# Kernel tuning notes

Hardware: AMD Instinct MI355X
Metric: run time of the kernel (lower is better)

Reference implementation:

```python
import jax, jax.numpy as jnp
import numpy as np

B, C, H, W = 64, 10, 30, 30
D, NH, HD = 64, 4, 16
EPS = 1e-5


def _conv(x, w, b):
    # x: [B,Cin,H,W], w: [Cout,Cin,kh,kw] (OIHW), SAME padding, stride 1
    y = jax.lax.conv_general_dilated(x, w, (1, 1), 'SAME',
                                     dimension_numbers=('NCHW', 'OIHW', 'NCHW'))
    return y + b[None, :, None, None]


def setup_inputs() -> dict:
    key = jax.random.key(0)
    ks = jax.random.split(key, 20)
    inp = {}
    inp['input_grid'] = jax.random.uniform(ks[0], (B, C, H, W), dtype=jnp.float32)
    inp['embed'] = jax.random.normal(ks[1], (10, D), dtype=jnp.float32)
    # MultiheadAttention packed in_proj [3D, D] and out_proj [D, D]
    inp['in_proj_w'] = jax.random.normal(ks[2], (3 * D, D), dtype=jnp.float32) * 0.08
    inp['in_proj_b'] = jnp.zeros((3 * D,), dtype=jnp.float32)
    inp['out_proj_w'] = jax.random.normal(ks[3], (D, D), dtype=jnp.float32) * 0.08
    inp['out_proj_b'] = jnp.zeros((D,), dtype=jnp.float32)
    # spatial encoder convs
    inp['conv1_w'] = jax.random.normal(ks[4], (32, 10, 3, 3), dtype=jnp.float32) * 0.1
    inp['conv1_b'] = jnp.zeros((32,), dtype=jnp.float32)
    inp['conv2_w'] = jax.random.normal(ks[5], (64, 32, 3, 3), dtype=jnp.float32) * 0.06
    inp['conv2_b'] = jnp.zeros((64,), dtype=jnp.float32)
    # color mapper MLP 64 -> 128 -> 100
    inp['lin1_w'] = jax.random.normal(ks[6], (128, 64), dtype=jnp.float32) * 0.1
    inp['lin1_b'] = jnp.zeros((128,), dtype=jnp.float32)
    inp['lin2_w'] = jax.random.normal(ks[7], (100, 128), dtype=jnp.float32) * 0.08
    inp['lin2_b'] = jnp.zeros((100,), dtype=jnp.float32)
    # decoder: ConvTranspose2d(64,32,3,pad=1) weight is [in=64,out=32,3,3]
    inp['dec1_w'] = jax.random.normal(ks[8], (64, 32, 3, 3), dtype=jnp.float32) * 0.06
    inp['dec1_b'] = jnp.zeros((32,), dtype=jnp.float32)
    inp['bn_g'] = jnp.ones((32,), dtype=jnp.float32)
    inp['bn_b'] = jnp.zeros((32,), dtype=jnp.float32)
    # ConvTranspose2d(32,10,1) weight [in=32,out=10,1,1] -> store as [32,10]
    inp['dec2_w'] = jax.random.normal(ks[9], (32, 10), dtype=jnp.float32) * 0.26
    inp['dec2_b'] = jnp.array([0.0, 0.08, 0.06, 0.07, 0.05, 0.06, 0.08, 0.09, 0.07, 0.06],
                              dtype=jnp.float32)
    return inp


def reference(input_grid, embed, in_proj_w, in_proj_b, out_proj_w, out_proj_b,
              conv1_w, conv1_b, conv2_w, conv2_b,
              lin1_w, lin1_b, lin2_w, lin2_b,
              dec1_w, dec1_b, bn_g, bn_b, dec2_w, dec2_b):
    b, c, h, w = input_grid.shape
    L = h * w
    idx = jnp.argmax(input_grid, axis=1)                      # [B,H,W] int
    x = embed[idx].reshape(b, L, D)                           # [B,L,64]

    # self-attention (torch MHA semantics, avg attn weights over heads)
    qkv = x @ in_proj_w.T + in_proj_b                         # [B,L,3D]
    q, k, v = jnp.split(qkv, 3, axis=-1)
    def heads(t):
        return t.reshape(b, L, NH, HD).transpose(0, 2, 1, 3)  # [B,NH,L,HD]
    q, k, v = heads(q), heads(k), heads(v)
    scores = jnp.einsum('bhqd,bhkd->bhqk', q, k) / np.sqrt(HD)
    attn = jax.nn.softmax(scores, axis=-1)                    # [B,NH,L,L]
    color_weights = attn.mean(axis=1)                         # [B,L,L]
    ctx = jnp.einsum('bhqk,bhkd->bhqd', attn, v)
    ctx = ctx.transpose(0, 2, 1, 3).reshape(b, L, D)
    attended = ctx @ out_proj_w.T + out_proj_b                # [B,L,64]
    attended_sp = attended.reshape(b, h, w, D).transpose(0, 3, 1, 2)  # [B,64,H,W]

    # spatial encoder
    s = jax.nn.relu(_conv(input_grid, conv1_w, conv1_b))
    s = jax.nn.relu(_conv(s, conv2_w, conv2_b))
    combined = s + attended_sp                                # [B,64,H,W]

    # global pool -> color map logits
    gf = combined.mean(axis=(2, 3))                           # [B,64]
    hmid = jax.nn.relu(gf @ lin1_w.T + lin1_b)
    color_map_logits = (hmid @ lin2_w.T + lin2_b).reshape(b, 10, 10)

    # vectorized color remap (replaces the per-batch/per-color scatter loop)
    new_color = jnp.argmax(color_map_logits, axis=-1)         # [B,10]
    pix = jnp.take_along_axis(new_color, idx.reshape(b, L), axis=1).reshape(b, h, w)
    mapped_output = jax.nn.one_hot(pix, 10, dtype=input_grid.dtype)
    mapped_output = mapped_output.transpose(0, 3, 1, 2)       # [B,10,H,W]

    # decoder: convT(64->32,k3,p1,s1) == conv with flipped kernel, SAME
    w1 = jnp.flip(dec1_w, axis=(2, 3)).transpose(1, 0, 2, 3)  # [32,64,3,3] OIHW
    d = _conv(combined, w1, dec1_b)
    # BatchNorm2d eval mode: running_mean=0, running_var=1
    d = d / np.sqrt(1.0 + EPS) * bn_g[None, :, None, None] + bn_b[None, :, None, None]
    d = jax.nn.relu(d)                                        # Dropout2d inactive (inference)
    predicted_output = jnp.einsum('bihw,io->bohw', d, dec2_w) + dec2_b[None, :, None, None]

    color_map = jax.nn.softmax(color_map_logits, axis=-1)
    return predicted_output, color_map, color_weights, mapped_output
```

## Files before the change

### kernel.cpp

```cpp
#include <hip/hip_runtime.h>
#include <cstddef>

#define B 64
#define NC 10
#define L 900
#define STASH_STRIDE 36000

typedef float f32x4 __attribute__((ext_vector_type(4)));

#define SCR_COMB   0
#define SCR_S1     3686400
#define SCR_AT     5529600
#define SCR_VE     5570560
#define SCR_S      5571200
#define SCR_WT2    5571600
#define SCR_WT1    5590032
#define SCR_BIAS1  5608464
#define SCR_GFP    5608496
#define SCR_CNT    5669936
#define SCR_FLOATS 5670576

__global__ __launch_bounds__(256) void k_front(
    const float* __restrict__ g, const float* __restrict__ embed,
    const float* __restrict__ ipw, const float* __restrict__ ipb,
    const float* __restrict__ cw1, const float* __restrict__ c1b,
    const float* __restrict__ cw2, const float* __restrict__ dw,
    const float* __restrict__ db, const float* __restrict__ bng,
    const float* __restrict__ bnb,
    float* __restrict__ scr, unsigned char* __restrict__ stash) {
  int bid = blockIdx.x, t = threadIdx.x;
  __shared__ float smem[4352];
  if (bid == 0) {
    float* emb = smem; float* q = smem + 640; float* k = smem + 1280;
    float* ve = scr + SCR_VE; float* S = scr + SCR_S;
    for (int i = t; i < 640; i += 256) emb[i] = embed[i];
    __syncthreads();
    for (int row = t; row < 192; row += 256) {
      int which = row >> 6, d = row & 63;
      for (int c = 0; c < 10; ++c) {
        float acc = ipb[row];
        for (int j = 0; j < 64; ++j) acc += emb[c * 64 + j] * ipw[row * 64 + j];
        if (which == 0) q[c * 64 + d] = acc;
        else if (which == 1) k[c * 64 + d] = acc;
        else ve[c * 64 + d] = acc;
      }
    }
    __syncthreads();
    for (int i = t; i < 400; i += 256) {
      int h = i / 100, r = i % 100, cq = r / 10, ck = r % 10;
      float acc = 0.f;
      for (int e = 0; e < 16; ++e)
        acc += q[cq * 64 + h * 16 + e] * k[ck * 64 + h * 16 + e];
      S[i] = acc * 0.25f;
    }
  } else if (bid <= 145) {
    int i = (bid - 1) * 256 + t;
    if (i < 18432) {
      int r = i / 64, oc = i % 64;
      scr[SCR_WT2 + r * 64 + oc] = cw2[oc * 288 + r];
    } else if (i < 36864) {
      int e = i - 18432, r = e / 32, oc = e % 32;
      int ic = r / 9, kk = r % 9, ky = kk / 3, kx = kk % 3;
      float s = bng[oc] / sqrtf(1.f + 1e-5f);
      scr[SCR_WT1 + r * 32 + oc] = dw[((ic * 32 + oc) * 3 + (2 - ky)) * 3 + (2 - kx)] * s;
    } else if (i < 36896) {
      int oc = i - 36864;
      float s = bng[oc] / sqrtf(1.f + 1e-5f);
      scr[SCR_BIAS1 + oc] = db[oc] * s + bnb[oc];
    }
  } else if (bid <= 209) {
    int b = bid - 146;
    int* hist = (int*)smem;
    int* cnt = (int*)(scr + SCR_CNT);
    if (t < 10) hist[t] = 0;
    __syncthreads();
    const float* gb = g + (size_t)b * NC * L;
    int* sidx = (int*)(stash + (size_t)b * STASH_STRIDE);
    for (int p = t; p < L; p += 256) {
      float best = gb[p]; int bi = 0;
      for (int c = 1; c < NC; ++c) {
        float v = gb[c * L + p];
        if (v > best) { best = v; bi = c; }
      }
      sidx[p] = bi;
      atomicAdd(&hist[bi], 1);
    }
    __syncthreads();
    if (t < 10) cnt[b * NC + t] = hist[t];
  } else {
    int blk = bid - 210, b = blk / 15, pr = blk % 15, oh0 = pr * 2;
    float* ins = smem;
    float* ws = smem + 1360;
    float* s1 = scr + SCR_S1;
    for (int i = t; i < 2880; i += 256) ws[i] = cw1[i];
    for (int e = t; e < 1360; e += 256) {
      int r = e / 340, rem = e % 340, ic = rem / 34, x = rem % 34;
      int y = oh0 + r - 1, gx = x - 1;
      float v = 0.f;
      if (y >= 0 && y < 30 && gx >= 0 && gx < 30)
        v = g[(size_t)(b * 10 + ic) * 900 + y * 30 + gx];
      ins[(r * 10 + ic) * 34 + x] = v;
    }
    __syncthreads();
    int lane = t & 63, ow = lane & 31, rr = lane >> 5;
    int oc0 = __builtin_amdgcn_readfirstlane((t >> 6) * 8);
    float acc[8];
    #pragma unroll
    for (int j = 0; j < 8; ++j) acc[j] = c1b[oc0 + j];
    for (int ic = 0; ic < 10; ++ic) {
      #pragma unroll
      for (int ky = 0; ky < 3; ++ky) {
        #pragma unroll
        for (int kx = 0; kx < 3; ++kx) {
          float iv = ins[((rr + ky) * 10 + ic) * 34 + ow + kx];
          #pragma unroll
          for (int j = 0; j < 8; ++j)
            acc[j] = fmaf(iv, ws[((oc0 + j) * 10 + ic) * 9 + ky * 3 + kx], acc[j]);
        }
      }
    }
    if (ow < 30) {
      #pragma unroll
      for (int j = 0; j < 8; ++j)
        s1[(size_t)(b * 32 + oc0 + j) * 900 + (oh0 + rr) * 30 + ow] = fmaxf(acc[j], 0.f);
    }
  }
}

__global__ void k_attn(const float* __restrict__ S, const float* __restrict__ ve,
                       const int* __restrict__ cnt,
                       const float* __restrict__ opw, const float* __restrict__ opb,
                       float* __restrict__ AT, unsigned char* __restrict__ stash) {
  int b = blockIdx.x, t = threadIdx.x;
  float* scw = (float*)(stash + (size_t)b * STASH_STRIDE + 3640);
  __shared__ float A[4][10][10];
  __shared__ float cf[10];
  __shared__ float ctx[10][64];
  if (t < 10) cf[t] = (float)cnt[b * 10 + t];
  __syncthreads();
  if (t < 40) {
    int h = t / 10, cq = t % 10;
    const float* Sr = S + (h * 10 + cq) * 10;
    float m = -1e30f;
    for (int c = 0; c < 10; ++c) if (cf[c] > 0.f) m = fmaxf(m, Sr[c]);
    float e[10]; float Z = 0.f;
    for (int c = 0; c < 10; ++c) { e[c] = expf(Sr[c] - m); Z += cf[c] * e[c]; }
    float inv = 1.f / Z;
    for (int c = 0; c < 10; ++c) A[h][cq][c] = e[c] * inv;
  }
  __syncthreads();
  if (t < 100) {
    int cq = t / 10, ck = t % 10;
    scw[t] = 0.25f * (A[0][cq][ck] + A[1][cq][ck] + A[2][cq][ck] + A[3][cq][ck]);
  }
  for (int i = t; i < 640; i += 128) {
    int cq = i >> 6, dd = i & 63, h = dd >> 4;
    float acc = 0.f;
    for (int ck = 0; ck < 10; ++ck) acc += A[h][cq][ck] * cf[ck] * ve[ck * 64 + dd];
    ctx[cq][dd] = acc;
  }
  __syncthreads();
  for (int i = t; i < 640; i += 128) {
    int cq = i >> 6, dd = i & 63;
    float acc = opb[dd];
    for (int e = 0; e < 64; ++e) acc += ctx[cq][e] * opw[dd * 64 + e];
    AT[(b * 10 + cq) * 64 + dd] = acc;
  }
}

__global__ __launch_bounds__(256) void k_c2(const float* __restrict__ scr_s1,
                                            const float* __restrict__ wt2,
                                            const float* __restrict__ cb,
                                            const float* __restrict__ AT,
                                            const unsigned char* __restrict__ stash,
                                            float* __restrict__ comb,
                                            float* __restrict__ gfp) {
  int blk = blockIdx.x, b = blk / 15, pr = blk % 15, oh0 = pr * 2;
  int t = threadIdx.x;
  __shared__ float ins[4][32][34];
  for (int e = t; e < 4352; e += 256) {
    int r = e / 1088, rem = e % 1088, ic = rem / 34, x = rem % 34;
    int y = oh0 + r - 1, gx = x - 1;
    float v = 0.f;
    if (y >= 0 && y < 30 && gx >= 0 && gx < 30)
      v = scr_s1[(size_t)(b * 32 + ic) * 900 + y * 30 + gx];
    ins[r][ic][x] = v;
  }
  __syncthreads();
  int lane = t & 63, ow = lane & 31, rr = lane >> 5;
  int oc0 = __builtin_amdgcn_readfirstlane((t >> 6) * 16);
  float acc[16];
  #pragma unroll
  for (int j = 0; j < 16; ++j) acc[j] = cb[oc0 + j];
  for (int ic = 0; ic < 32; ++ic) {
    #pragma unroll
    for (int ky = 0; ky < 3; ++ky) {
      #pragma unroll
      for (int kx = 0; kx < 3; ++kx) {
        float iv = ins[rr + ky][ic][ow + kx];
        const float* wr = wt2 + (ic * 9 + ky * 3 + kx) * 64 + oc0;
        #pragma unroll
        for (int j = 0; j < 16; ++j) acc[j] = fmaf(iv, wr[j], acc[j]);
      }
    }
  }
  float outv[16];
  if (ow < 30) {
    const int* sidx = (const int*)(stash + (size_t)b * STASH_STRIDE);
    int c = sidx[(oh0 + rr) * 30 + ow];
    const float* at = AT + ((size_t)b * 10 + c) * 64 + oc0;
    #pragma unroll
    for (int j = 0; j < 16; ++j) {
      outv[j] = fmaxf(acc[j], 0.f) + at[j];
      comb[(size_t)(b * 64 + oc0 + j) * 900 + (oh0 + rr) * 30 + ow] = outv[j];
    }
  } else {
    #pragma unroll
    for (int j = 0; j < 16; ++j) outv[j] = 0.f;
  }
  #pragma unroll
  for (int j = 0; j < 16; ++j) {
    float v = outv[j];
    for (int o = 32; o; o >>= 1) v += __shfl_down(v, o, 64);
    if (lane == 0) gfp[(b * 15 + pr) * 64 + oc0 + j] = v;
  }
}

__global__ __launch_bounds__(256) void k_back(
    const float* __restrict__ scr,
    const float* __restrict__ l1w, const float* __restrict__ l1b,
    const float* __restrict__ l2w, const float* __restrict__ l2b,
    const float* __restrict__ w2, const float* __restrict__ b2,
    float* __restrict__ out_pred, float* __restrict__ out_cm,
    float* __restrict__ out_cw2, unsigned char* __restrict__ stash) {
  int bid = blockIdx.x, t = threadIdx.x;
  __shared__ float smem[10880];
  if (bid < 64) {
    int b = bid;
    float* gfl = smem; float* hmid = smem + 64; float* lg = smem + 192;
    const float* gfp = scr + SCR_GFP;
    if (t < 64) {
      float a = 0.f;
      for (int pr = 0; pr < 15; ++pr) a += gfp[(b * 15 + pr) * 64 + t];
      gfl[t] = a * (1.f / 900.f);
    }
    __syncthreads();
    if (t < 128) {
      float acc = l1b[t];
      for (int j = 0; j < 64; ++j) acc += gfl[j] * l1w[t * 64 + j];
      hmid[t] = fmaxf(acc, 0.f);
    }
    __syncthreads();
    if (t < 100) {
      float acc = l2b[t];
      for (int j = 0; j < 128; ++j) acc += hmid[j] * l2w[t * 128 + j];
      lg[t] = acc;
    }
    __syncthreads();
    if (t < 10) {
      float m = lg[t * 10]; int am = 0;
      for (int j = 1; j < 10; ++j) {
        float v = lg[t * 10 + j];
        if (v > m) { m = v; am = j; }
      }
      float e[10]; float Z = 0.f;
      for (int j = 0; j < 10; ++j) { e[j] = expf(lg[t * 10 + j] - m); Z += e[j]; }
      float inv = 1.f / Z;
      for (int j = 0; j < 10; ++j) out_cm[(b * 10 + t) * 10 + j] = e[j] * inv;
      ((int*)(stash + (size_t)b * STASH_STRIDE + 3600))[t] = am;
    }
  } else if (bid < 1024) {
    int blk = bid - 64, b = blk / 15, pr = blk % 15, oh0 = pr * 2;
    float* ins = smem;
    float* d1s = smem + 8704;
    const float* comb = scr + SCR_COMB;
    const float* wt1 = scr + SCR_WT1;
    const float* bias1 = scr + SCR_BIAS1;
    for (int e = t; e < 8704; e += 256) {
      int r = e / 2176, rem = e % 2176, ic = rem / 34, x = rem % 34;
      int y = oh0 + r - 1, gx = x - 1;
      float v = 0.f;
      if (y >= 0 && y < 30 && gx >= 0 && gx < 30)
        v = comb[(size_t)(b * 64 + ic) * 900 + y * 30 + gx];
      ins[(r * 64 + ic) * 34 + x] = v;
    }
    __syncthreads();
    int lane = t & 63, ow = lane & 31, rr = lane >> 5;
    int oc0 = __builtin_amdgcn_readfirstlane((t >> 6) * 8);
    float acc[8];
    #pragma unroll
    for (int j = 0; j < 8; ++j) acc[j] = bias1[oc0 + j];
    for (int ic = 0; ic < 64; ++ic) {
      #pragma unroll
      for (int ky = 0; ky < 3; ++ky) {
        #pragma unroll
        for (int kx = 0; kx < 3; ++kx) {
          float iv = ins[((rr + ky) * 64 + ic) * 34 + ow + kx];
          const float* wr = wt1 + (ic * 9 + ky * 3 + kx) * 32 + oc0;
          #pragma unroll
          for (int j = 0; j < 8; ++j) acc[j] = fmaf(iv, wr[j], acc[j]);
        }
      }
    }
    if (ow < 30) {
      #pragma unroll
      for (int j = 0; j < 8; ++j) d1s[(rr * 32 + oc0 + j) * 32 + ow] = fmaxf(acc[j], 0.f);
    }
    __syncthreads();
    for (int e = t; e < 600; e += 256) {
      int r = e / 300, rem = e % 300, o = rem / 30, ow2 = rem % 30;
      float a2 = b2[o];
      #pragma unroll
      for (int ic = 0; ic < 32; ++ic) a2 += d1s[(r * 32 + ic) * 32 + ow2] * w2[ic * 10 + o];
      out_pred[(size_t)(b * 10 + o) * 900 + (oh0 + r) * 30 + ow2] = a2;
    }
  } else {
    int blk = bid - 1024, b = blk / 60, rc = blk % 60;
    float* lut = smem;
    float* cwb = smem + 9000;
    unsigned char* cols = (unsigned char*)(smem + 9100);
    const unsigned char* sl = stash + (size_t)b * STASH_STRIDE;
    const int* sidx = (const int*)sl;
    const float* scw = (const float*)(sl + 3640);
    for (int i = t; i < 900; i += 256) cols[i] = (unsigned char)sidx[i];
    for (int i = t; i < 100; i += 256) cwb[i] = scw[i];
    __syncthreads();
    for (int i = t; i < 9000; i += 256) {
      int cq = i / 900, p = i % 900;
      lut[cq * 900 + p] = cwb[cq * 10 + cols[p]];
    }
    __syncthreads();
    int base = rc * 15;
    for (int i = t; i < 15 * 225; i += 256) {
      int r = i / 225, ch = i % 225;
      int p = base + r;
      int cq = cols[p];
      f32x4 v = *(const f32x4*)&lut[cq * 900 + ch * 4];
      __builtin_nontemporal_store(v, (f32x4*)&out_cw2[(size_t)b * 810000 + (size_t)p * 900 + ch * 4]);
    }
  }
}

__global__ void k_cw(const unsigned char* __restrict__ stash,
                     float* __restrict__ out2) {
  int blk = blockIdx.x;
  int b = blk / 60, rc = blk % 60;
  int t = threadIdx.x;
  const unsigned char* sl = stash + (size_t)b * STASH_STRIDE;
  const int* sidx = (const int*)sl;
  const float* scw = (const float*)(sl + 3640);
  __shared__ float lut[10][900];
  __shared__ unsigned char cols[900];
  __shared__ float cwb[100];
  for (int i = t; i < 900; i += 256) cols[i] = (unsigned char)sidx[i];
  for (int i = t; i < 100; i += 256) cwb[i] = scw[i];
  __syncthreads();
  for (int i = t; i < 9000; i += 256) {
    int cq = i / 900, p = i % 900;
    lut[cq][p] = cwb[cq * 10 + cols[p]];
  }
  __syncthreads();
  int base = rc * 15;
  for (int i = t; i < 15 * 225; i += 256) {
    int r = i / 225, ch = i % 225;
    int p = base + r;
    int cq = cols[p];
    f32x4 v = *(const f32x4*)&lut[cq][ch * 4];
    __builtin_nontemporal_store(v, (f32x4*)&out2[(size_t)b * 810000 + (size_t)p * 900 + ch * 4]);
  }
}

__global__ void k_map(const unsigned char* __restrict__ stash,
                      float* __restrict__ out4) {
  int b = blockIdx.x, t = threadIdx.x;
  const unsigned char* sl = stash + (size_t)b * STASH_STRIDE;
  const int* sidx = (const int*)sl;
  const int* sncol = (const int*)(sl + 3600);
  __shared__ unsigned char scol[900];
  __shared__ int sn[10];
  for (int i = t; i < 900; i += 256) scol[i] = (unsigned char)sidx[i];
  if (t < 10) sn[t] = sncol[t];
  __syncthreads();
  for (int i = t; i < 9000; i += 256) {
    int ch = i / 900, p = i % 900;
    out4[(size_t)b * 9000 + i] = (sn[scol[p]] == ch) ? 1.0f : 0.0f;
  }
}

extern "C" void kernel_launch(void* const* d_in, const int* in_sizes, int n_in,
                              void* d_out, int out_size, void* d_ws, size_t ws_size,
                              hipStream_t stream) {
  const float* input_grid = (const float*)d_in[0];
  const float* embed      = (const float*)d_in[1];
  const float* in_proj_w  = (const float*)d_in[2];
  const float* in_proj_b  = (const float*)d_in[3];
  const float* out_proj_w = (const float*)d_in[4];
  const float* out_proj_b = (const float*)d_in[5];
  const float* conv1_w    = (const float*)d_in[6];
  const float* conv1_b    = (const float*)d_in[7];
  const float* conv2_w    = (const float*)d_in[8];
  const float* conv2_b    = (const float*)d_in[9];
  const float* lin1_w     = (const float*)d_in[10];
  const float* lin1_b     = (const float*)d_in[11];
  const float* lin2_w     = (const float*)d_in[12];
  const float* lin2_b     = (const float*)d_in[13];
  const float* dec1_w     = (const float*)d_in[14];
  const float* dec1_b     = (const float*)d_in[15];
  const float* bn_g       = (const float*)d_in[16];
  const float* bn_b       = (const float*)d_in[17];
  const float* dec2_w     = (const float*)d_in[18];
  const float* dec2_b     = (const float*)d_in[19];

  float* out      = (float*)d_out;
  float* out_pred = out;
  float* out_cmap = out + 576000;
  float* out_cw   = out + 582400;
  float* out_map  = out + 52422400;

  bool ws_ok = ws_size >= (size_t)SCR_FLOATS * 4;
  float* scr = ws_ok ? (float*)d_ws : out_cw;
  unsigned char* stash = (unsigned char*)out_map;

  k_front<<<1170, 256, 0, stream>>>(input_grid, embed, in_proj_w, in_proj_b,
                                    conv1_w, conv1_b, conv2_w, dec1_w, dec1_b,
                                    bn_g, bn_b, scr, stash);
  k_attn<<<B, 128, 0, stream>>>(scr + SCR_S, scr + SCR_VE, (int*)(scr + SCR_CNT),
                                out_proj_w, out_proj_b, scr + SCR_AT, stash);
  k_c2<<<960, 256, 0, stream>>>(scr + SCR_S1, scr + SCR_WT2, conv2_b,
                                scr + SCR_AT, stash, scr + SCR_COMB, scr + SCR_GFP);
  k_back<<<ws_ok ? 4864 : 1024, 256, 0, stream>>>(scr, lin1_w, lin1_b, lin2_w, lin2_b,
                                                  dec2_w, dec2_b, out_pred, out_cmap,
                                                  out_cw, stash);
  if (!ws_ok) k_cw<<<B * 60, 256, 0, stream>>>(stash, out_cw);
  k_map<<<B, 256, 0, stream>>>(stash, out_map);
}
```

Baseline: 179.3 us.

## Fuse attention into conv2 kernel and mapped-output into back kernel

The per-batch attention work is folded into the conv2 kernel: each conv2 block recomputes its batch's softmax, context and output projection into shared memory instead of reading a separate AT buffer. A new branch in k_back recomputes the colour-mapper MLP argmax and writes the one-hot mapped output, so k_map is dropped. The workspace layout is reorganised, with s1 placed in the color_weights output region and the stash moved into the workspace. The default path goes from five launches to three, at the cost of redundant attention math in every conv2 block (15x per batch) and a duplicated MLP.

```diff
diff --git a/kernel.cpp b/kernel.cpp
--- a/kernel.cpp
+++ b/kernel.cpp
@@ -4,21 +4,8 @@
 #define B 64
 #define NC 10
 #define L 900
-#define STASH_STRIDE 36000
 
 typedef float f32x4 __attribute__((ext_vector_type(4)));
-
-#define SCR_COMB   0
-#define SCR_S1     3686400
-#define SCR_AT     5529600
-#define SCR_VE     5570560
-#define SCR_S      5571200
-#define SCR_WT2    5571600
-#define SCR_WT1    5590032
-#define SCR_BIAS1  5608464
-#define SCR_GFP    5608496
-#define SCR_CNT    5669936
-#define SCR_FLOATS 5670576
 
 __global__ __launch_bounds__(256) void k_front(
     const float* __restrict__ g, const float* __restrict__ embed,
@@ -27,12 +14,15 @@
     const float* __restrict__ cw2, const float* __restrict__ dw,
     const float* __restrict__ db, const float* __restrict__ bng,
     const float* __restrict__ bnb,
-    float* __restrict__ scr, unsigned char* __restrict__ stash) {
+    float* __restrict__ ve_g, float* __restrict__ S_g,
+    float* __restrict__ wt2, float* __restrict__ wt1,
+    float* __restrict__ bias1, int* __restrict__ cnt,
+    float* __restrict__ s1, unsigned char* __restrict__ stash,
+    int sstride) {
   int bid = blockIdx.x, t = threadIdx.x;
   __shared__ float smem[4352];
   if (bid == 0) {
     float* emb = smem; float* q = smem + 640; float* k = smem + 1280;
-    float* ve = scr + SCR_VE; float* S = scr + SCR_S;
     for (int i = t; i < 640; i += 256) emb[i] = embed[i];
     __syncthreads();
     for (int row = t; row < 192; row += 256) {
@@ -42,7 +32,7 @@
         for (int j = 0; j < 64; ++j) acc += emb[c * 64 + j] * ipw[row * 64 + j];
         if (which == 0) q[c * 64 + d] = acc;
         else if (which == 1) k[c * 64 + d] = acc;
-        else ve[c * 64 + d] = acc;
+        else ve_g[c * 64 + d] = acc;
       }
     }
     __syncthreads();
@@ -51,31 +41,30 @@
       float acc = 0.f;
       for (int e = 0; e < 16; ++e)
         acc += q[cq * 64 + h * 16 + e] * k[ck * 64 + h * 16 + e];
-      S[i] = acc * 0.25f;
+      S_g[i] = acc * 0.25f;
     }
   } else if (bid <= 145) {
     int i = (bid - 1) * 256 + t;
     if (i < 18432) {
       int r = i / 64, oc = i % 64;
-      scr[SCR_WT2 + r * 64 + oc] = cw2[oc * 288 + r];
+      wt2[r * 64 + oc] = cw2[oc * 288 + r];
     } else if (i < 36864) {
       int e = i - 18432, r = e / 32, oc = e % 32;
       int ic = r / 9, kk = r % 9, ky = kk / 3, kx = kk % 3;
       float s = bng[oc] / sqrtf(1.f + 1e-5f);
-      scr[SCR_WT1 + r * 32 + oc] = dw[((ic * 32 + oc) * 3 + (2 - ky)) * 3 + (2 - kx)] * s;
+      wt1[r * 32 + oc] = dw[((ic * 32 + oc) * 3 + (2 - ky)) * 3 + (2 - kx)] * s;
     } else if (i < 36896) {
       int oc = i - 36864;
       float s = bng[oc] / sqrtf(1.f + 1e-5f);
-      scr[SCR_BIAS1 + oc] = db[oc] * s + bnb[oc];
+      bias1[oc] = db[oc] * s + bnb[oc];
     }
   } else if (bid <= 209) {
     int b = bid - 146;
     int* hist = (int*)smem;
-    int* cnt = (int*)(scr + SCR_CNT);
     if (t < 10) hist[t] = 0;
     __syncthreads();
     const float* gb = g + (size_t)b * NC * L;
-    int* sidx = (int*)(stash + (size_t)b * STASH_STRIDE);
+    int* sidx = (int*)(stash + (size_t)b * sstride);
     for (int p = t; p < L; p += 256) {
       float best = gb[p]; int bi = 0;
       for (int c = 1; c < NC; ++c) {
@@ -91,7 +80,6 @@
     int blk = bid - 210, b = blk / 15, pr = blk % 15, oh0 = pr * 2;
     float* ins = smem;
     float* ws = smem + 1360;
-    float* s1 = scr + SCR_S1;
     for (int i = t; i < 2880; i += 256) ws[i] = cw1[i];
     for (int e = t; e < 1360; e += 256) {
       int r = e / 340, rem = e % 340, ic = rem / 34, x = rem % 34;
@@ -127,15 +115,28 @@
   }
 }
 
-__global__ void k_attn(const float* __restrict__ S, const float* __restrict__ ve,
-                       const int* __restrict__ cnt,
-                       const float* __restrict__ opw, const float* __restrict__ opb,
-                       float* __restrict__ AT, unsigned char* __restrict__ stash) {
-  int b = blockIdx.x, t = threadIdx.x;
-  float* scw = (float*)(stash + (size_t)b * STASH_STRIDE + 3640);
+__global__ __launch_bounds__(256) void k_c2attn(
+    const float* __restrict__ s1, const float* __restrict__ wt2,
+    const float* __restrict__ cb, const float* __restrict__ S,
+    const float* __restrict__ ve, const int* __restrict__ cnt,
+    const float* __restrict__ opw, const float* __restrict__ opb,
+    unsigned char* __restrict__ stash, int sstride,
+    float* __restrict__ comb, float* __restrict__ gfp) {
+  int blk = blockIdx.x, b = blk / 15, pr = blk % 15, oh0 = pr * 2;
+  int t = threadIdx.x;
+  __shared__ float ins[4][32][34];
   __shared__ float A[4][10][10];
   __shared__ float cf[10];
-  __shared__ float ctx[10][64];
+  __shared__ float ctx[10][65];
+  __shared__ float at[10][65];
+  for (int e = t; e < 4352; e += 256) {
+    int r = e / 1088, rem = e % 1088, ic = rem / 34, x = rem % 34;
+    int y = oh0 + r - 1, gx = x - 1;
+    float v = 0.f;
+    if (y >= 0 && y < 30 && gx >= 0 && gx < 30)
+      v = s1[(size_t)(b * 32 + ic) * 900 + y * 30 + gx];
+    ins[r][ic][x] = v;
+  }
   if (t < 10) cf[t] = (float)cnt[b * 10 + t];
   __syncthreads();
   if (t < 40) {
@@ -151,6 +152,86 @@
   __syncthreads();
   if (t < 100) {
     int cq = t / 10, ck = t % 10;
+    float* scw = (float*)(stash + (size_t)b * sstride + 3640);
+    scw[t] = 0.25f * (A[0][cq][ck] + A[1][cq][ck] + A[2][cq][ck] + A[3][cq][ck]);
+  }
+  for (int i = t; i < 640; i += 256) {
+    int cq = i >> 6, dd = i & 63, h = dd >> 4;
+    float acc = 0.f;
+    for (int ck = 0; ck < 10; ++ck) acc += A[h][cq][ck] * cf[ck] * ve[ck * 64 + dd];
+    ctx[cq][dd] = acc;
+  }
+  __syncthreads();
+  for (int i = t; i < 640; i += 256) {
+    int cq = i >> 6, dd = i & 63;
+    float acc = opb[dd];
+    for (int e = 0; e < 64; ++e) acc += ctx[cq][e] * opw[dd * 64 + e];
+    at[cq][dd] = acc;
+  }
+  __syncthreads();
+  int lane = t & 63, ow = lane & 31, rr = lane >> 5;
+  int oc0 = __builtin_amdgcn_readfirstlane((t >> 6) * 16);
+  float acc[16];
+  #pragma unroll
+  for (int j = 0; j < 16; ++j) acc[j] = cb[oc0 + j];
+  for (int ic = 0; ic < 32; ++ic) {
+    #pragma unroll
+    for (int ky = 0; ky < 3; ++ky) {
+      #pragma unroll
+      for (int kx = 0; kx < 3; ++kx) {
+        float iv = ins[rr + ky][ic][ow + kx];
+        const float* wr = wt2 + (ic * 9 + ky * 3 + kx) * 64 + oc0;
+        #pragma unroll
+        for (int j = 0; j < 16; ++j) acc[j] = fmaf(iv, wr[j], acc[j]);
+      }
+    }
+  }
+  float outv[16];
+  if (ow < 30) {
+    const int* sidx = (const int*)(stash + (size_t)b * sstride);
+    int c = sidx[(oh0 + rr) * 30 + ow];
+    #pragma unroll
+    for (int j = 0; j < 16; ++j) {
+      outv[j] = fmaxf(acc[j], 0.f) + at[c][oc0 + j];
+      comb[(size_t)(b * 64 + oc0 + j) * 900 + (oh0 + rr) * 30 + ow] = outv[j];
+    }
+  } else {
+    #pragma unroll
+    for (int j = 0; j < 16; ++j) outv[j] = 0.f;
+  }
+  #pragma unroll
+  for (int j = 0; j < 16; ++j) {
+    float v = outv[j];
+    for (int o = 32; o; o >>= 1) v += __shfl_down(v, o, 64);
+    if (lane == 0) gfp[(b * 15 + pr) * 64 + oc0 + j] = v;
+  }
+}
+
+__global__ void k_attn(const float* __restrict__ S, const float* __restrict__ ve,
+                       const int* __restrict__ cnt,
+                       const float* __restrict__ opw, const float* __restrict__ opb,
+                       float* __restrict__ AT, unsigned char* __restrict__ stash,
+                       int sstride) {
+  int b = blockIdx.x, t = threadIdx.x;
+  float* scw = (float*)(stash + (size_t)b * sstride + 3640);
+  __shared__ float A[4][10][10];
+  __shared__ float cf[10];
+  __shared__ float ctx[10][64];
+  if (t < 10) cf[t] = (float)cnt[b * 10 + t];
+  __syncthreads();
+  if (t < 40) {
+    int h = t / 10, cq = t % 10;
+    const float* Sr = S + (h * 10 + cq) * 10;
+    float m = -1e30f;
+    for (int c = 0; c < 10; ++c) if (cf[c] > 0.f) m = fmaxf(m, Sr[c]);
+    float e[10]; float Z = 0.f;
+    for (int c = 0; c < 10; ++c) { e[c] = expf(Sr[c] - m); Z += cf[c] * e[c]; }
+    float inv = 1.f / Z;
+    for (int c = 0; c < 10; ++c) A[h][cq][c] = e[c] * inv;
+  }
+  __syncthreads();
+  if (t < 100) {
+    int cq = t / 10, ck = t % 10;
     scw[t] = 0.25f * (A[0][cq][ck] + A[1][cq][ck] + A[2][cq][ck] + A[3][cq][ck]);
   }
   for (int i = t; i < 640; i += 128) {
@@ -168,11 +249,12 @@
   }
 }
 
-__global__ __launch_bounds__(256) void k_c2(const float* __restrict__ scr_s1,
+__global__ __launch_bounds__(256) void k_c2(const float* __restrict__ s1,
                                             const float* __restrict__ wt2,
                                             const float* __restrict__ cb,
                                             const float* __restrict__ AT,
                                             const unsigned char* __restrict__ stash,
+                                            int sstride,
                                             float* __restrict__ comb,
                                             float* __restrict__ gfp) {
   int blk = blockIdx.x, b = blk / 15, pr = blk % 15, oh0 = pr * 2;
@@ -183,7 +265,7 @@
     int y = oh0 + r - 1, gx = x - 1;
     float v = 0.f;
     if (y >= 0 && y < 30 && gx >= 0 && gx < 30)
-      v = scr_s1[(size_t)(b * 32 + ic) * 900 + y * 30 + gx];
+      v = s1[(size_t)(b * 32 + ic) * 900 + y * 30 + gx];
     ins[r][ic][x] = v;
   }
   __syncthreads();
@@ -206,12 +288,12 @@
   }
   float outv[16];
   if (ow < 30) {
-    const int* sidx = (const int*)(stash + (size_t)b * STASH_STRIDE);
+    const int* sidx = (const int*)(stash + (size_t)b * sstride);
     int c = sidx[(oh0 + rr) * 30 + ow];
-    const float* at = AT + ((size_t)b * 10 + c) * 64 + oc0;
+    const float* atp = AT + ((size_t)b * 10 + c) * 64 + oc0;
     #pragma unroll
     for (int j = 0; j < 16; ++j) {
-      outv[j] = fmaxf(acc[j], 0.f) + at[j];
+      outv[j] = fmaxf(acc[j], 0.f) + atp[j];
       comb[(size_t)(b * 64 + oc0 + j) * 900 + (oh0 + rr) * 30 + ow] = outv[j];
     }
   } else {
@@ -227,18 +309,19 @@
 }
 
 __global__ __launch_bounds__(256) void k_back(
-    const float* __restrict__ scr,
+    const float* __restrict__ comb, const float* __restrict__ wt1,
+    const float* __restrict__ bias1, const float* __restrict__ gfp,
     const float* __restrict__ l1w, const float* __restrict__ l1b,
     const float* __restrict__ l2w, const float* __restrict__ l2b,
     const float* __restrict__ w2, const float* __restrict__ b2,
     float* __restrict__ out_pred, float* __restrict__ out_cm,
-    float* __restrict__ out_cw2, unsigned char* __restrict__ stash) {
+    float* __restrict__ out_cw2, float* __restrict__ out_map,
+    unsigned char* __restrict__ stash, int sstride) {
   int bid = blockIdx.x, t = threadIdx.x;
   __shared__ float smem[10880];
   if (bid < 64) {
     int b = bid;
     float* gfl = smem; float* hmid = smem + 64; float* lg = smem + 192;
-    const float* gfp = scr + SCR_GFP;
     if (t < 64) {
       float a = 0.f;
       for (int pr = 0; pr < 15; ++pr) a += gfp[(b * 15 + pr) * 64 + t];
@@ -267,15 +350,12 @@
       for (int j = 0; j < 10; ++j) { e[j] = expf(lg[t * 10 + j] - m); Z += e[j]; }
       float inv = 1.f / Z;
       for (int j = 0; j < 10; ++j) out_cm[(b * 10 + t) * 10 + j] = e[j] * inv;
-      ((int*)(stash + (size_t)b * STASH_STRIDE + 3600))[t] = am;
+      ((int*)(stash + (size_t)b * sstride + 3600))[t] = am;
     }
   } else if (bid < 1024) {
     int blk = bid - 64, b = blk / 15, pr = blk % 15, oh0 = pr * 2;
     float* ins = smem;
     float* d1s = smem + 8704;
-    const float* comb = scr + SCR_COMB;
-    const float* wt1 = scr + SCR_WT1;
-    const float* bias1 = scr + SCR_BIAS1;
     for (int e = t; e < 8704; e += 256) {
       int r = e / 2176, rem = e % 2176, ic = rem / 34, x = rem % 34;
       int y = oh0 + r - 1, gx = x - 1;
@@ -314,12 +394,12 @@
       for (int ic = 0; ic < 32; ++ic) a2 += d1s[(r * 32 + ic) * 32 + ow2] * w2[ic * 10 + o];
       out_pred[(size_t)(b * 10 + o) * 900 + (oh0 + r) * 30 + ow2] = a2;
     }
-  } else {
+  } else if (bid < 4864) {
     int blk = bid - 1024, b = blk / 60, rc = blk % 60;
     float* lut = smem;
     float* cwb = smem + 9000;
     unsigned char* cols = (unsigned char*)(smem + 9100);
-    const unsigned char* sl = stash + (size_t)b * STASH_STRIDE;
+    const unsigned char* sl = stash + (size_t)b * sstride;
     const int* sidx = (const int*)sl;
     const float* scw = (const float*)(sl + 3640);
     for (int i = t; i < 900; i += 256) cols[i] = (unsigned char)sidx[i];
@@ -338,15 +418,53 @@
       f32x4 v = *(const f32x4*)&lut[cq * 900 + ch * 4];
       __builtin_nontemporal_store(v, (f32x4*)&out_cw2[(size_t)b * 810000 + (size_t)p * 900 + ch * 4]);
     }
-  }
-}
-
-__global__ void k_cw(const unsigned char* __restrict__ stash,
+  } else {
+    int b = bid - 4864;
+    float* gfl = smem; float* hmid = smem + 64; float* lg = smem + 192;
+    int* sn = (int*)(smem + 292);
+    unsigned char* scol = (unsigned char*)(smem + 302);
+    const int* sidx = (const int*)(stash + (size_t)b * sstride);
+    for (int i = t; i < 900; i += 256) scol[i] = (unsigned char)sidx[i];
+    if (t < 64) {
+      float a = 0.f;
+      for (int pr = 0; pr < 15; ++pr) a += gfp[(b * 15 + pr) * 64 + t];
+      gfl[t] = a * (1.f / 900.f);
+    }
+    __syncthreads();
+    if (t < 128) {
+      float acc = l1b[t];
+      for (int j = 0; j < 64; ++j) acc += gfl[j] * l1w[t * 64 + j];
+      hmid[t] = fmaxf(acc, 0.f);
+    }
+    __syncthreads();
+    if (t < 100) {
+      float acc = l2b[t];
+      for (int j = 0; j < 128; ++j) acc += hmid[j] * l2w[t * 128 + j];
+      lg[t] = acc;
+    }
+    __syncthreads();
+    if (t < 10) {
+      float m = lg[t * 10]; int am = 0;
+      for (int j = 1; j < 10; ++j) {
+        float v = lg[t * 10 + j];
+        if (v > m) { m = v; am = j; }
+      }
+      sn[t] = am;
+    }
+    __syncthreads();
+    for (int i = t; i < 9000; i += 256) {
+      int ch = i / 900, p = i % 900;
+      out_map[(size_t)b * 9000 + i] = (sn[scol[p]] == ch) ? 1.0f : 0.0f;
+    }
+  }
+}
+
+__global__ void k_cw(const unsigned char* __restrict__ stash, int sstride,
                      float* __restrict__ out2) {
   int blk = blockIdx.x;
   int b = blk / 60, rc = blk % 60;
   int t = threadIdx.x;
-  const unsigned char* sl = stash + (size_t)b * STASH_STRIDE;
+  const unsigned char* sl = stash + (size_t)b * sstride;
   const int* sidx = (const int*)sl;
   const float* scw = (const float*)(sl + 3640);
   __shared__ float lut[10][900];
@@ -370,10 +488,10 @@
   }
 }
 
-__global__ void k_map(const unsigned char* __restrict__ stash,
+__global__ void k_map(const unsigned char* __restrict__ stash, int sstride,
                       float* __restrict__ out4) {
   int b = blockIdx.x, t = threadIdx.x;
-  const unsigned char* sl = stash + (size_t)b * STASH_STRIDE;
+  const unsigned char* sl = stash + (size_t)b * sstride;
   const int* sidx = (const int*)sl;
   const int* sncol = (const int*)(sl + 3600);
   __shared__ unsigned char scol[900];
@@ -417,20 +535,59 @@
   float* out_cw   = out + 582400;
   float* out_map  = out + 52422400;
 
-  bool ws_ok = ws_size >= (size_t)SCR_FLOATS * 4;
-  float* scr = ws_ok ? (float*)d_ws : out_cw;
-  unsigned char* stash = (unsigned char*)out_map;
-
-  k_front<<<1170, 256, 0, stream>>>(input_grid, embed, in_proj_w, in_proj_b,
-                                    conv1_w, conv1_b, conv2_w, dec1_w, dec1_b,
-                                    bn_g, bn_b, scr, stash);
-  k_attn<<<B, 128, 0, stream>>>(scr + SCR_S, scr + SCR_VE, (int*)(scr + SCR_CNT),
-                                out_proj_w, out_proj_b, scr + SCR_AT, stash);
-  k_c2<<<960, 256, 0, stream>>>(scr + SCR_S1, scr + SCR_WT2, conv2_b,
-                                scr + SCR_AT, stash, scr + SCR_COMB, scr + SCR_GFP);
-  k_back<<<ws_ok ? 4864 : 1024, 256, 0, stream>>>(scr, lin1_w, lin1_b, lin2_w, lin2_b,
-                                                  dec2_w, dec2_b, out_pred, out_cmap,
-                                                  out_cw, stash);
-  if (!ws_ok) k_cw<<<B * 60, 256, 0, stream>>>(stash, out_cw);
-  k_map<<<B, 256, 0, stream>>>(stash, out_map);
-}
+  const size_t WS_NEED = (size_t)(3786416 + 65536) * 4;
+  bool ws_ok = ws_size >= WS_NEED;
+
+  if (ws_ok) {
+    float* w = (float*)d_ws;
+    float* comb  = w;
+    float* ve    = w + 3686400;
+    float* S     = w + 3687040;
+    float* wt2   = w + 3687440;
+    float* wt1   = w + 3705872;
+    float* bias1 = w + 3724304;
+    float* gfp   = w + 3724336;
+    int*   cnt   = (int*)(w + 3785776);
+    unsigned char* stash = (unsigned char*)(w + 3786416);
+    float* s1 = out_cw;
+
+    k_front<<<1170, 256, 0, stream>>>(input_grid, embed, in_proj_w, in_proj_b,
+                                      conv1_w, conv1_b, conv2_w, dec1_w, dec1_b,
+                                      bn_g, bn_b, ve, S, wt2, wt1, bias1, cnt,
+                                      s1, stash, 4096);
+    k_c2attn<<<960, 256, 0, stream>>>(s1, wt2, conv2_b, S, ve, cnt,
+                                      out_proj_w, out_proj_b, stash, 4096,
+                                      comb, gfp);
+    k_back<<<4928, 256, 0, stream>>>(comb, wt1, bias1, gfp, lin1_w, lin1_b,
+                                     lin2_w, lin2_b, dec2_w, dec2_b,
+                                     out_pred, out_cmap, out_cw, out_map,
+                                     stash, 4096);
+  } else {
+    float* scr = out_cw;
+    float* comb  = scr;
+    float* s1    = scr + 3686400;
+    float* AT    = scr + 5529600;
+    float* ve    = scr + 5570560;
+    float* S     = scr + 5571200;
+    float* wt2   = scr + 5571600;
+    float* wt1   = scr + 5590032;
+    float* bias1 = scr + 5608464;
+    float* gfp   = scr + 5608496;
+    int*   cnt   = (int*)(scr + 5669936);
+    unsigned char* stash = (unsigned char*)out_map;
+
+    k_front<<<1170, 256, 0, stream>>>(input_grid, embed, in_proj_w, in_proj_b,
+                                      conv1_w, conv1_b, conv2_w, dec1_w, dec1_b,
+                                      bn_g, bn_b, ve, S, wt2, wt1, bias1, cnt,
+                                      s1, stash, 36000);
+    k_attn<<<B, 128, 0, stream>>>(S, ve, cnt, out_proj_w, out_proj_b, AT,
+                                  stash, 36000);
+    k_c2<<<960, 256, 0, stream>>>(s1, wt2, conv2_b, AT, stash, 36000, comb, gfp);
+    k_back<<<1024, 256, 0, stream>>>(comb, wt1, bias1, gfp, lin1_w, lin1_b,
+                                     lin2_w, lin2_b, dec2_w, dec2_b,
+                                     out_pred, out_cmap, out_cw, out_map,
+                                     stash, 36000);
+    k_cw<<<B * 60, 256, 0, stream>>>(stash, 36000, out_cw);
+    k_map<<<B, 256, 0, stream>>>(stash, 36000, out_map);
+  }
+}
```

After: 180.1 us. No clear change (+0.5%).

## Fuse attention into conv2, recompute color weights per block, merge tail kernels

Applied to the files above, without the earlier changes.

The per-batch attention kernel is folded into the conv2 kernel, and each block now recomputes the attention context it needs into shared memory. The color-weight broadcast blocks recompute argmax, histogram, QK scores and softmax themselves instead of reading stashed values. They are interleaved with the decoder blocks in k_back, and the map output is computed there too. Scratch now lives in the tail of the color-weight output region, which is overwritten last by a separate tail kernel. This cuts kernel launches and dependencies and overlaps write-heavy work with decoder compute, at the cost of redundant recomputation in every block and an ordering dependence on scratch aliasing.

```diff
diff --git a/kernel.cpp b/kernel.cpp
--- a/kernel.cpp
+++ b/kernel.cpp
@@ -4,21 +4,101 @@
 #define B 64
 #define NC 10
 #define L 900
-#define STASH_STRIDE 36000
+#define SSTRIDE 36000
 
 typedef float f32x4 __attribute__((ext_vector_type(4)));
 
 #define SCR_COMB   0
 #define SCR_S1     3686400
-#define SCR_AT     5529600
-#define SCR_VE     5570560
-#define SCR_S      5571200
-#define SCR_WT2    5571600
-#define SCR_WT1    5590032
-#define SCR_BIAS1  5608464
-#define SCR_GFP    5608496
-#define SCR_CNT    5669936
-#define SCR_FLOATS 5670576
+#define SCR_VE     5529600
+#define SCR_S      5530240
+#define SCR_WT2    5530640
+#define SCR_WT1    5549072
+#define SCR_BIAS1  5567504
+#define SCR_GFP    5567536
+#define SCR_CNT    5628976
+
+__device__ __forceinline__ void cw_block(int b, int rc,
+                                         const float* __restrict__ g,
+                                         const float* __restrict__ embed,
+                                         const float* __restrict__ ipw,
+                                         const float* __restrict__ ipb,
+                                         float* __restrict__ out_cw,
+                                         float* sm) {
+  float* qs = sm;
+  float* ks = sm + 640;
+  float* Sl = sm + 1280;
+  float* lut = sm + 1680;
+  float* emb = sm + 1680;
+  float* cwb = sm + 10680;
+  float* cf = sm + 10780;
+  int* hist = (int*)(sm + 10790);
+  unsigned char* cols = (unsigned char*)(sm + 10800);
+  int t = threadIdx.x;
+  for (int i = t; i < 640; i += 256) emb[i] = embed[i];
+  if (t < 10) hist[t] = 0;
+  __syncthreads();
+  {
+    int row = t & 127, c0 = (t >> 7) * 5;
+    const float* wrow = ipw + row * 64;
+    float bias = ipb[row];
+    for (int c = c0; c < c0 + 5; ++c) {
+      float acc = bias;
+      for (int j = 0; j < 64; ++j) acc += emb[c * 64 + j] * wrow[j];
+      if (row < 64) qs[c * 64 + row] = acc;
+      else ks[c * 64 + (row - 64)] = acc;
+    }
+  }
+  const float* gb = g + (size_t)b * NC * L;
+  for (int p = t; p < 900; p += 256) {
+    float best = gb[p]; int bi = 0;
+    for (int c = 1; c < NC; ++c) {
+      float v = gb[c * L + p];
+      if (v > best) { best = v; bi = c; }
+    }
+    cols[p] = (unsigned char)bi;
+    atomicAdd(&hist[bi], 1);
+  }
+  __syncthreads();
+  for (int i = t; i < 400; i += 256) {
+    int h = i / 100, r = i % 100, cq = r / 10, ck = r % 10;
+    float acc = 0.f;
+    for (int e = 0; e < 16; ++e)
+      acc += qs[cq * 64 + h * 16 + e] * ks[ck * 64 + h * 16 + e];
+    Sl[i] = acc * 0.25f;
+  }
+  if (t < 10) cf[t] = (float)hist[t];
+  __syncthreads();
+  float* Al = qs;
+  if (t < 40) {
+    int h = t / 10, cq = t % 10;
+    const float* Sr = Sl + h * 100 + cq * 10;
+    float m = -1e30f;
+    for (int c = 0; c < 10; ++c) if (cf[c] > 0.f) m = fmaxf(m, Sr[c]);
+    float e[10]; float Z = 0.f;
+    for (int c = 0; c < 10; ++c) { e[c] = expf(Sr[c] - m); Z += cf[c] * e[c]; }
+    float inv = 1.f / Z;
+    for (int c = 0; c < 10; ++c) Al[(h * 10 + cq) * 10 + c] = e[c] * inv;
+  }
+  __syncthreads();
+  if (t < 100) {
+    cwb[t] = 0.25f * (Al[t] + Al[100 + t] + Al[200 + t] + Al[300 + t]);
+  }
+  __syncthreads();
+  for (int i = t; i < 9000; i += 256) {
+    int cq = i / 900, p = i % 900;
+    lut[cq * 900 + p] = cwb[cq * 10 + cols[p]];
+  }
+  __syncthreads();
+  int base = rc * 15;
+  for (int i = t; i < 15 * 225; i += 256) {
+    int r = i / 225, ch = i % 225;
+    int p = base + r;
+    int cq = cols[p];
+    f32x4 v = *(const f32x4*)&lut[cq * 900 + ch * 4];
+    __builtin_nontemporal_store(v, (f32x4*)&out_cw[(size_t)b * 810000 + (size_t)p * 900 + ch * 4]);
+  }
+}
 
 __global__ __launch_bounds__(256) void k_front(
     const float* __restrict__ g, const float* __restrict__ embed,
@@ -32,7 +112,6 @@
   __shared__ float smem[4352];
   if (bid == 0) {
     float* emb = smem; float* q = smem + 640; float* k = smem + 1280;
-    float* ve = scr + SCR_VE; float* S = scr + SCR_S;
     for (int i = t; i < 640; i += 256) emb[i] = embed[i];
     __syncthreads();
     for (int row = t; row < 192; row += 256) {
@@ -42,7 +121,7 @@
         for (int j = 0; j < 64; ++j) acc += emb[c * 64 + j] * ipw[row * 64 + j];
         if (which == 0) q[c * 64 + d] = acc;
         else if (which == 1) k[c * 64 + d] = acc;
-        else ve[c * 64 + d] = acc;
+        else scr[SCR_VE + c * 64 + d] = acc;
       }
     }
     __syncthreads();
@@ -51,7 +130,7 @@
       float acc = 0.f;
       for (int e = 0; e < 16; ++e)
         acc += q[cq * 64 + h * 16 + e] * k[ck * 64 + h * 16 + e];
-      S[i] = acc * 0.25f;
+      scr[SCR_S + i] = acc * 0.25f;
     }
   } else if (bid <= 145) {
     int i = (bid - 1) * 256 + t;
@@ -75,7 +154,7 @@
     if (t < 10) hist[t] = 0;
     __syncthreads();
     const float* gb = g + (size_t)b * NC * L;
-    int* sidx = (int*)(stash + (size_t)b * STASH_STRIDE);
+    int* sidx = (int*)(stash + (size_t)b * SSTRIDE);
     for (int p = t; p < L; p += 256) {
       float best = gb[p]; int bi = 0;
       for (int c = 1; c < NC; ++c) {
@@ -127,15 +206,30 @@
   }
 }
 
-__global__ void k_attn(const float* __restrict__ S, const float* __restrict__ ve,
-                       const int* __restrict__ cnt,
-                       const float* __restrict__ opw, const float* __restrict__ opb,
-                       float* __restrict__ AT, unsigned char* __restrict__ stash) {
-  int b = blockIdx.x, t = threadIdx.x;
-  float* scw = (float*)(stash + (size_t)b * STASH_STRIDE + 3640);
+__global__ __launch_bounds__(256) void k_c2attn(
+    const float* __restrict__ scr_in, const float* __restrict__ cb,
+    const float* __restrict__ opw, const float* __restrict__ opb,
+    const unsigned char* __restrict__ stash,
+    float* __restrict__ scr) {
+  int blk = blockIdx.x, b = blk / 15, pr = blk % 15, oh0 = pr * 2;
+  int t = threadIdx.x;
+  const float* s1 = scr_in + SCR_S1;
+  const float* S = scr_in + SCR_S;
+  const float* ve = scr_in + SCR_VE;
+  const int* cnt = (const int*)(scr_in + SCR_CNT);
+  __shared__ float ins[4][32][34];
   __shared__ float A[4][10][10];
   __shared__ float cf[10];
-  __shared__ float ctx[10][64];
+  __shared__ float ctx[10][65];
+  __shared__ float at[10][65];
+  for (int e = t; e < 4352; e += 256) {
+    int r = e / 1088, rem = e % 1088, ic = rem / 34, x = rem % 34;
+    int y = oh0 + r - 1, gx = x - 1;
+    float v = 0.f;
+    if (y >= 0 && y < 30 && gx >= 0 && gx < 30)
+      v = s1[(size_t)(b * 32 + ic) * 900 + y * 30 + gx];
+    ins[r][ic][x] = v;
+  }
   if (t < 10) cf[t] = (float)cnt[b * 10 + t];
   __syncthreads();
   if (t < 40) {
@@ -149,42 +243,18 @@
     for (int c = 0; c < 10; ++c) A[h][cq][c] = e[c] * inv;
   }
   __syncthreads();
-  if (t < 100) {
-    int cq = t / 10, ck = t % 10;
-    scw[t] = 0.25f * (A[0][cq][ck] + A[1][cq][ck] + A[2][cq][ck] + A[3][cq][ck]);
-  }
-  for (int i = t; i < 640; i += 128) {
+  for (int i = t; i < 640; i += 256) {
     int cq = i >> 6, dd = i & 63, h = dd >> 4;
     float acc = 0.f;
     for (int ck = 0; ck < 10; ++ck) acc += A[h][cq][ck] * cf[ck] * ve[ck * 64 + dd];
     ctx[cq][dd] = acc;
   }
   __syncthreads();
-  for (int i = t; i < 640; i += 128) {
+  for (int i = t; i < 640; i += 256) {
     int cq = i >> 6, dd = i & 63;
     float acc = opb[dd];
     for (int e = 0; e < 64; ++e) acc += ctx[cq][e] * opw[dd * 64 + e];
-    AT[(b * 10 + cq) * 64 + dd] = acc;
-  }
-}
-
-__global__ __launch_bounds__(256) void k_c2(const float* __restrict__ scr_s1,
-                                            const float* __restrict__ wt2,
-                                            const float* __restrict__ cb,
-                                            const float* __restrict__ AT,
-                                            const unsigned char* __restrict__ stash,
-                                            float* __restrict__ comb,
-                                            float* __restrict__ gfp) {
-  int blk = blockIdx.x, b = blk / 15, pr = blk % 15, oh0 = pr * 2;
-  int t = threadIdx.x;
-  __shared__ float ins[4][32][34];
-  for (int e = t; e < 4352; e += 256) {
-    int r = e / 1088, rem = e % 1088, ic = rem / 34, x = rem % 34;
-    int y = oh0 + r - 1, gx = x - 1;
-    float v = 0.f;
-    if (y >= 0 && y < 30 && gx >= 0 && gx < 30)
-      v = scr_s1[(size_t)(b * 32 + ic) * 900 + y * 30 + gx];
-    ins[r][ic][x] = v;
+    at[cq][dd] = acc;
   }
   __syncthreads();
   int lane = t & 63, ow = lane & 31, rr = lane >> 5;
@@ -192,6 +262,7 @@
   float acc[16];
   #pragma unroll
   for (int j = 0; j < 16; ++j) acc[j] = cb[oc0 + j];
+  const float* wt2 = scr_in + SCR_WT2;
   for (int ic = 0; ic < 32; ++ic) {
     #pragma unroll
     for (int ky = 0; ky < 3; ++ky) {
@@ -205,13 +276,13 @@
     }
   }
   float outv[16];
+  float* comb = scr + SCR_COMB;
   if (ow < 30) {
-    const int* sidx = (const int*)(stash + (size_t)b * STASH_STRIDE);
+    const int* sidx = (const int*)(stash + (size_t)b * SSTRIDE);
     int c = sidx[(oh0 + rr) * 30 + ow];
-    const float* at = AT + ((size_t)b * 10 + c) * 64 + oc0;
     #pragma unroll
     for (int j = 0; j < 16; ++j) {
-      outv[j] = fmaxf(acc[j], 0.f) + at[j];
+      outv[j] = fmaxf(acc[j], 0.f) + at[c][oc0 + j];
       comb[(size_t)(b * 64 + oc0 + j) * 900 + (oh0 + rr) * 30 + ow] = outv[j];
     }
   } else {
@@ -222,55 +293,33 @@
   for (int j = 0; j < 16; ++j) {
     float v = outv[j];
     for (int o = 32; o; o >>= 1) v += __shfl_down(v, o, 64);
-    if (lane == 0) gfp[(b * 15 + pr) * 64 + oc0 + j] = v;
+    if (lane == 0) scr[SCR_GFP + (b * 15 + pr) * 64 + oc0 + j] = v;
   }
 }
 
 __global__ __launch_bounds__(256) void k_back(
+    const float* __restrict__ g, const float* __restrict__ embed,
+    const float* __restrict__ ipw, const float* __restrict__ ipb,
     const float* __restrict__ scr,
     const float* __restrict__ l1w, const float* __restrict__ l1b,
     const float* __restrict__ l2w, const float* __restrict__ l2b,
     const float* __restrict__ w2, const float* __restrict__ b2,
     float* __restrict__ out_pred, float* __restrict__ out_cm,
-    float* __restrict__ out_cw2, unsigned char* __restrict__ stash) {
+    float* __restrict__ out_cw2, float* __restrict__ out_map,
+    unsigned char* __restrict__ stash) {
   int bid = blockIdx.x, t = threadIdx.x;
-  __shared__ float smem[10880];
-  if (bid < 64) {
-    int b = bid;
-    float* gfl = smem; float* hmid = smem + 64; float* lg = smem + 192;
-    const float* gfp = scr + SCR_GFP;
-    if (t < 64) {
-      float a = 0.f;
-      for (int pr = 0; pr < 15; ++pr) a += gfp[(b * 15 + pr) * 64 + t];
-      gfl[t] = a * (1.f / 900.f);
-    }
-    __syncthreads();
-    if (t < 128) {
-      float acc = l1b[t];
-      for (int j = 0; j < 64; ++j) acc += gfl[j] * l1w[t * 64 + j];
-      hmid[t] = fmaxf(acc, 0.f);
-    }
-    __syncthreads();
-    if (t < 100) {
-      float acc = l2b[t];
-      for (int j = 0; j < 128; ++j) acc += hmid[j] * l2w[t * 128 + j];
-      lg[t] = acc;
-    }
-    __syncthreads();
-    if (t < 10) {
-      float m = lg[t * 10]; int am = 0;
-      for (int j = 1; j < 10; ++j) {
-        float v = lg[t * 10 + j];
-        if (v > m) { m = v; am = j; }
-      }
-      float e[10]; float Z = 0.f;
-      for (int j = 0; j < 10; ++j) { e[j] = expf(lg[t * 10 + j] - m); Z += e[j]; }
-      float inv = 1.f / Z;
-      for (int j = 0; j < 10; ++j) out_cm[(b * 10 + t) * 10 + j] = e[j] * inv;
-      ((int*)(stash + (size_t)b * STASH_STRIDE + 3600))[t] = am;
-    }
-  } else if (bid < 1024) {
-    int blk = bid - 64, b = blk / 15, pr = blk % 15, oh0 = pr * 2;
+  __shared__ float smem[11100];
+  int cwid = -1, d1id = -1;
+  if (bid < 3840) {
+    if ((bid & 3) == 3) d1id = bid >> 2;
+    else cwid = (bid >> 2) * 3 + (bid & 3);
+  } else if (bid < 4320) {
+    cwid = 2880 + (bid - 3840);
+  }
+  if (cwid >= 0) {
+    cw_block(cwid / 60, cwid % 60, g, embed, ipw, ipb, out_cw2, smem);
+  } else if (d1id >= 0) {
+    int b = d1id / 15, pr = d1id % 15, oh0 = pr * 2;
     float* ins = smem;
     float* d1s = smem + 8704;
     const float* comb = scr + SCR_COMB;
@@ -314,77 +363,85 @@
       for (int ic = 0; ic < 32; ++ic) a2 += d1s[(r * 32 + ic) * 32 + ow2] * w2[ic * 10 + o];
       out_pred[(size_t)(b * 10 + o) * 900 + (oh0 + r) * 30 + ow2] = a2;
     }
+  } else if (bid < 4384) {
+    int b = bid - 4320;
+    float* gfl = smem; float* hmid = smem + 64; float* lg = smem + 192;
+    const float* gfp = scr + SCR_GFP;
+    if (t < 64) {
+      float a = 0.f;
+      for (int pr = 0; pr < 15; ++pr) a += gfp[(b * 15 + pr) * 64 + t];
+      gfl[t] = a * (1.f / 900.f);
+    }
+    __syncthreads();
+    if (t < 128) {
+      float acc = l1b[t];
+      for (int j = 0; j < 64; ++j) acc += gfl[j] * l1w[t * 64 + j];
+      hmid[t] = fmaxf(acc, 0.f);
+    }
+    __syncthreads();
+    if (t < 100) {
+      float acc = l2b[t];
+      for (int j = 0; j < 128; ++j) acc += hmid[j] * l2w[t * 128 + j];
+      lg[t] = acc;
+    }
+    __syncthreads();
+    if (t < 10) {
+      float m = lg[t * 10];
+      for (int j = 1; j < 10; ++j) m = fmaxf(m, lg[t * 10 + j]);
+      float e[10]; float Z = 0.f;
+      for (int j = 0; j < 10; ++j) { e[j] = expf(lg[t * 10 + j] - m); Z += e[j]; }
+      float inv = 1.f / Z;
+      for (int j = 0; j < 10; ++j) out_cm[(b * 10 + t) * 10 + j] = e[j] * inv;
+    }
   } else {
-    int blk = bid - 1024, b = blk / 60, rc = blk % 60;
-    float* lut = smem;
-    float* cwb = smem + 9000;
-    unsigned char* cols = (unsigned char*)(smem + 9100);
-    const unsigned char* sl = stash + (size_t)b * STASH_STRIDE;
-    const int* sidx = (const int*)sl;
-    const float* scw = (const float*)(sl + 3640);
-    for (int i = t; i < 900; i += 256) cols[i] = (unsigned char)sidx[i];
-    for (int i = t; i < 100; i += 256) cwb[i] = scw[i];
+    int b = bid - 4384;
+    float* gfl = smem; float* hmid = smem + 64; float* lg = smem + 192;
+    int* sn = (int*)(smem + 292);
+    unsigned char* scol = (unsigned char*)(smem + 302);
+    const float* gfp = scr + SCR_GFP;
+    const int* sidx = (const int*)(stash + (size_t)b * SSTRIDE);
+    for (int i = t; i < 900; i += 256) scol[i] = (unsigned char)sidx[i];
+    if (t < 64) {
+      float a = 0.f;
+      for (int pr = 0; pr < 15; ++pr) a += gfp[(b * 15 + pr) * 64 + t];
+      gfl[t] = a * (1.f / 900.f);
+    }
+    __syncthreads();
+    if (t < 128) {
+      float acc = l1b[t];
+      for (int j = 0; j < 64; ++j) acc += gfl[j] * l1w[t * 64 + j];
+      hmid[t] = fmaxf(acc, 0.f);
+    }
+    __syncthreads();
+    if (t < 100) {
+      float acc = l2b[t];
+      for (int j = 0; j < 128; ++j) acc += hmid[j] * l2w[t * 128 + j];
+      lg[t] = acc;
+    }
+    __syncthreads();
+    if (t < 10) {
+      float m = lg[t * 10]; int am = 0;
+      for (int j = 1; j < 10; ++j) {
+        float v = lg[t * 10 + j];
+        if (v > m) { m = v; am = j; }
+      }
+      sn[t] = am;
+    }
     __syncthreads();
     for (int i = t; i < 9000; i += 256) {
-      int cq = i / 900, p = i % 900;
-      lut[cq * 900 + p] = cwb[cq * 10 + cols[p]];
-    }
-    __syncthreads();
-    int base = rc * 15;
-    for (int i = t; i < 15 * 225; i += 256) {
-      int r = i / 225, ch = i % 225;
-      int p = base + r;
-      int cq = cols[p];
-      f32x4 v = *(const f32x4*)&lut[cq * 900 + ch * 4];
-      __builtin_nontemporal_store(v, (f32x4*)&out_cw2[(size_t)b * 810000 + (size_t)p * 900 + ch * 4]);
-    }
-  }
-}
-
-__global__ void k_cw(const unsigned char* __restrict__ stash,
-                     float* __restrict__ out2) {
-  int blk = blockIdx.x;
-  int b = blk / 60, rc = blk % 60;
-  int t = threadIdx.x;
-  const unsigned char* sl = stash + (size_t)b * STASH_STRIDE;
-  const int* sidx = (const int*)sl;
-  const float* scw = (const float*)(sl + 3640);
-  __shared__ float lut[10][900];
-  __shared__ unsigned char cols[900];
-  __shared__ float cwb[100];
-  for (int i = t; i < 900; i += 256) cols[i] = (unsigned char)sidx[i];
-  for (int i = t; i < 100; i += 256) cwb[i] = scw[i];
-  __syncthreads();
-  for (int i = t; i < 9000; i += 256) {
-    int cq = i / 900, p = i % 900;
-    lut[cq][p] = cwb[cq * 10 + cols[p]];
-  }
-  __syncthreads();
-  int base = rc * 15;
-  for (int i = t; i < 15 * 225; i += 256) {
-    int r = i / 225, ch = i % 225;
-    int p = base + r;
-    int cq = cols[p];
-    f32x4 v = *(const f32x4*)&lut[cq][ch * 4];
-    __builtin_nontemporal_store(v, (f32x4*)&out2[(size_t)b * 810000 + (size_t)p * 900 + ch * 4]);
-  }
-}
-
-__global__ void k_map(const unsigned char* __restrict__ stash,
-                      float* __restrict__ out4) {
-  int b = blockIdx.x, t = threadIdx.x;
-  const unsigned char* sl = stash + (size_t)b * STASH_STRIDE;
-  const int* sidx = (const int*)sl;
-  const int* sncol = (const int*)(sl + 3600);
-  __shared__ unsigned char scol[900];
-  __shared__ int sn[10];
-  for (int i = t; i < 900; i += 256) scol[i] = (unsigned char)sidx[i];
-  if (t < 10) sn[t] = sncol[t];
-  __syncthreads();
-  for (int i = t; i < 9000; i += 256) {
-    int ch = i / 900, p = i % 900;
-    out4[(size_t)b * 9000 + i] = (sn[scol[p]] == ch) ? 1.0f : 0.0f;
-  }
+      int ch = i / 900, p = i % 900;
+      out_map[(size_t)b * 9000 + i] = (sn[scol[p]] == ch) ? 1.0f : 0.0f;
+    }
+  }
+}
+
+__global__ __launch_bounds__(256) void k_cwtail(
+    const float* __restrict__ g, const float* __restrict__ embed,
+    const float* __restrict__ ipw, const float* __restrict__ ipb,
+    float* __restrict__ out_cw2) {
+  __shared__ float smem[11100];
+  int bid = blockIdx.x;
+  cw_block(56 + bid / 60, bid % 60, g, embed, ipw, ipb, out_cw2, smem);
 }
 
 extern "C" void kernel_launch(void* const* d_in, const int* in_sizes, int n_in,
@@ -417,20 +474,18 @@
   float* out_cw   = out + 582400;
   float* out_map  = out + 52422400;
 
-  bool ws_ok = ws_size >= (size_t)SCR_FLOATS * 4;
-  float* scr = ws_ok ? (float*)d_ws : out_cw;
+  float* scr = out_cw + 46080000;
   unsigned char* stash = (unsigned char*)out_map;
 
   k_front<<<1170, 256, 0, stream>>>(input_grid, embed, in_proj_w, in_proj_b,
                                     conv1_w, conv1_b, conv2_w, dec1_w, dec1_b,
                                     bn_g, bn_b, scr, stash);
-  k_attn<<<B, 128, 0, stream>>>(scr + SCR_S, scr + SCR_VE, (int*)(scr + SCR_CNT),
-                                out_proj_w, out_proj_b, scr + SCR_AT, stash);
-  k_c2<<<960, 256, 0, stream>>>(scr + SCR_S1, scr + SCR_WT2, conv2_b,
-                                scr + SCR_AT, stash, scr + SCR_COMB, scr + SCR_GFP);
-  k_back<<<ws_ok ? 4864 : 1024, 256, 0, stream>>>(scr, lin1_w, lin1_b, lin2_w, lin2_b,
-                                                  dec2_w, dec2_b, out_pred, out_cmap,
-                                                  out_cw, stash);
-  if (!ws_ok) k_cw<<<B * 60, 256, 0, stream>>>(stash, out_cw);
-  k_map<<<B, 256, 0, stream>>>(stash, out_map);
-}
+  k_c2attn<<<960, 256, 0, stream>>>(scr, conv2_b, out_proj_w, out_proj_b,
+                                    stash, scr);
+  k_back<<<4448, 256, 0, stream>>>(input_grid, embed, in_proj_w, in_proj_b,
+                                   scr, lin1_w, lin1_b, lin2_w, lin2_b,
+                                   dec2_w, dec2_b, out_pred, out_cmap,
+                                   out_cw, out_map, stash);
+  k_cwtail<<<480, 256, 0, stream>>>(input_grid, embed, in_proj_w, in_proj_b,
+                                    out_cw);
+}
```

Measured after the change: 685.6 us. 282% more time.
